# Kernel optimization log

Hardware: AMD Instinct MI355X
Metric: run time of the kernel (lower is better)

Reference implementation:

```python
import jax, jax.numpy as jnp
import numpy as np

B, N, C, H = 4, 1024, 768, 12
D = C // H
SCALE = D ** -0.5


def setup_inputs() -> dict:
    key = jax.random.key(0)
    k1, k2, k3, k4 = jax.random.split(key, 4)
    x1 = jax.random.normal(k1, (B, N, C), dtype=jnp.float32)
    x2 = jax.random.normal(k2, (B, N, C), dtype=jnp.float32)
    # shared (dual-stream) Linear2 weights, torch nn.Linear layout: [out, in]
    W_qkv = jax.random.normal(k3, (3 * C, C), dtype=jnp.float32) * (C ** -0.5)
    b_qkv = jnp.zeros((3 * C,), dtype=jnp.float32)
    W_proj = jax.random.normal(k4, (C, C), dtype=jnp.float32) * (C ** -0.5)
    b_proj = jnp.zeros((C,), dtype=jnp.float32)
    return {"x1": x1, "x2": x2, "W_qkv": W_qkv, "b_qkv": b_qkv,
            "W_proj": W_proj, "b_proj": b_proj}


def _split_qkv(x, W_qkv, b_qkv):
    qkv = (x @ W_qkv.T + b_qkv).reshape(B, N, 3, H, D)
    qkv = jnp.transpose(qkv, (2, 0, 3, 1, 4))  # [3,B,H,N,D]
    return qkv[0], qkv[1], qkv[2]


def reference(x1, x2, W_qkv, b_qkv, W_proj, b_proj):
    q1, k1, v1 = _split_qkv(x1, W_qkv, b_qkv)
    q2, k2, v2 = _split_qkv(x2, W_qkv, b_qkv)
    # two score maps, combined before a single shared softmax
    s1 = jnp.einsum("bhqd,bhkd->bhqk", q1 * SCALE, k1)
    s2 = jnp.einsum("bhqd,bhkd->bhqk", q2 * SCALE, k2)
    attn = jax.nn.softmax(s1 + s2, axis=-1)  # [B,H,N,N]
    # same attention matrix applied to both value streams
    o1 = jnp.einsum("bhqk,bhkd->bhqd", attn, v1)
    o2 = jnpum = jnp.einsum("bhqk,bhkd->bhqd", attn, v2) if False else jnp.einsum("bhqk,bhkd->bhqd", attn, v2)
    o1 = jnp.transpose(o1, (0, 2, 1, 3)).reshape(B, N, C)
    o2 = jnp.transpose(o2, (0, 2, 1, 3)).reshape(B, N, C)
    y1 = o1 @ W_proj.T + b_proj
    y2 = o2 @ W_proj.T + b_proj
    return y1, y2
```

## Files before the change

kernel.cpp:

```cpp
#include <hip/hip_runtime.h>
#include <hip/hip_bf16.h>


typedef __bf16 bf16x8 __attribute__((ext_vector_type(8)));
typedef __bf16 bf16x4 __attribute__((ext_vector_type(4)));
typedef float  f32x4  __attribute__((ext_vector_type(4)));

__device__ __forceinline__ bf16x8 cvt8(const float* p) {
    f32x4 f0 = *(const f32x4*)p;
    f32x4 f1 = *(const f32x4*)(p + 4);
    bf16x8 r;
    r[0] = (__bf16)f0[0]; r[1] = (__bf16)f0[1]; r[2] = (__bf16)f0[2]; r[3] = (__bf16)f0[3];
    r[4] = (__bf16)f1[0]; r[5] = (__bf16)f1[1]; r[6] = (__bf16)f1[2]; r[7] = (__bf16)f1[3];
    return r;
}

__device__ __forceinline__ void async16(const __bf16* g, __bf16* l) {
    __builtin_amdgcn_global_load_lds(
        (const __attribute__((address_space(1))) void*)g,
        (__attribute__((address_space(3))) void*)l, 16, 0, 0);
}

__global__ __launch_bounds__(256)
void cvt4_k(const float* __restrict__ x1, const float* __restrict__ x2,
            const float* __restrict__ wq, const float* __restrict__ wp,
            __bf16* __restrict__ xc, __bf16* __restrict__ wqc,
            __bf16* __restrict__ wpc)
{
    int bid = blockIdx.x;
    const float* src; __bf16* dst; int i;
    if (bid < 1536)      { src = x1; dst = xc;             i = (bid * 256 + threadIdx.x) * 8; }
    else if (bid < 3072) { src = x2; dst = xc + 3145728;   i = ((bid - 1536) * 256 + threadIdx.x) * 8; }
    else if (bid < 3936) { src = wq; dst = wqc;            i = ((bid - 3072) * 256 + threadIdx.x) * 8; }
    else                 { src = wp; dst = wpc;            i = ((bid - 3936) * 256 + threadIdx.x) * 8; }
    *(bf16x8*)(dst + i) = cvt8(src + i);
}

__global__ __launch_bounds__(256)
void cvt_k(const float* __restrict__ src, __bf16* __restrict__ dst, int n) {
    int i = (blockIdx.x * 256 + threadIdx.x) * 8;
    if (i < n) *(bf16x8*)(dst + i) = cvt8(src + i);
}

__global__ __launch_bounds__(256)
void gemm_qkv_s(const __bf16* __restrict__ Xc, const __bf16* __restrict__ Wq,
                const float* __restrict__ bias,
                __bf16* __restrict__ qo, __bf16* __restrict__ ko,
                __bf16* __restrict__ vo)
{
    constexpr int K = 768;
    __shared__ __bf16 As[3][128 * 32];
    __shared__ __bf16 Bs[3][128 * 32];

    const int t = threadIdx.x, w = t >> 6, lane = t & 63;
    const int l15 = lane & 15, quad = lane >> 4;
    const int wm = w >> 1, wn = w & 1;

    const int bid  = blockIdx.x;
    const int xcd  = bid & 7;
    const int i6   = bid >> 3;
    const int pair = i6 / 18;
    const int gx   = i6 - pair * 18;
    const int p    = xcd * 8 + pair;
    const int gy   = p & 31;
    const int st   = p >> 5;

    const int sgrp = w * 32;
    const int srow = lane & 15;
    const int scol = (lane >> 4) * 8;

    const __bf16* Ab = Xc + (size_t)st * 3145728 + (size_t)(gy * 128) * K;
    const __bf16* Bb = Wq + (size_t)(gx * 128) * K;

    f32x4 acc[4][4];
#pragma unroll
    for (int mi = 0; mi < 4; mi++)
#pragma unroll
        for (int ni = 0; ni < 4; ni++) acc[mi][ni] = f32x4{0.f, 0.f, 0.f, 0.f};

#define QSTAGE(BUF, KT)                                                          \
    do {                                                                         \
        const int _k0 = (KT) * 32;                                               \
        async16(Ab + (size_t)(sgrp + srow) * K + _k0 + scol,                     \
                &As[BUF][sgrp * 32 + lane * 8]);                                 \
        async16(Ab + (size_t)(sgrp + 16 + srow) * K + _k0 + scol,                \
                &As[BUF][(sgrp + 16) * 32 + lane * 8]);                          \
        async16(Bb + (size_t)(sgrp + srow) * K + _k0 + scol,                     \
                &Bs[BUF][sgrp * 32 + lane * 8]);                                 \
        async16(Bb + (size_t)(sgrp + 16 + srow) * K + _k0 + scol,                \
                &Bs[BUF][(sgrp + 16) * 32 + lane * 8]);                          \
    } while (0)

    QSTAGE(0, 0);

#pragma unroll 3
    for (int kt = 0; kt < 24; kt++) {
        const int cb = kt % 3;
        if (kt < 23) {
            QSTAGE((kt + 1) % 3, kt + 1);
            asm volatile("s_waitcnt vmcnt(4)" ::: "memory");
        } else {
            asm volatile("s_waitcnt vmcnt(0)" ::: "memory");
        }
        __builtin_amdgcn_s_barrier();
        __builtin_amdgcn_sched_barrier(0);

        bf16x8 af[4], bfr[4];
#pragma unroll
        for (int mi = 0; mi < 4; mi++)
            af[mi] = *(const bf16x8*)&As[cb][(wm * 64 + mi * 16) * 32 + lane * 8];
#pragma unroll
        for (int ni = 0; ni < 4; ni++)
            bfr[ni] = *(const bf16x8*)&Bs[cb][(wn * 64 + ni * 16) * 32 + lane * 8];
#pragma unroll
        for (int mi = 0; mi < 4; mi++)
#pragma unroll
            for (int ni = 0; ni < 4; ni++)
                acc[mi][ni] = __builtin_amdgcn_mfma_f32_16x16x32_bf16(af[mi], bfr[ni], acc[mi][ni], 0, 0, 0);
    }
#undef QSTAGE

    const int which = (gx * 128) / 768;

    if (which == 2) {
#pragma unroll
        for (int ni = 0; ni < 4; ni++) {
            int j = gx * 128 + wn * 64 + ni * 16 + l15;
            int c = j - 1536;
            int h = c >> 6, d = c & 63;
            float bj = bias[j];
#pragma unroll
            for (int mi = 0; mi < 4; mi++) {
                int row0 = gy * 128 + wm * 64 + mi * 16 + quad * 4;
                int b = row0 >> 10, tok0 = row0 & 1023;
                bf16x4 pv;
#pragma unroll
                for (int r = 0; r < 4; r++) pv[r] = (__bf16)(acc[mi][ni][r] + bj);
                *(bf16x4*)&vo[((size_t)((st * 4 + b) * 12 + h) * 64 + d) * 1024 + tok0] = pv;
            }
        }
    } else {
#pragma unroll
        for (int ni = 0; ni < 4; ni++) {
            int j     = gx * 128 + wn * 64 + ni * 16 + l15;
            int c     = j - which * 768;
            int h = c >> 6, d = c & 63;
            float bj  = bias[j];
#pragma unroll
            for (int mi = 0; mi < 4; mi++) {
#pragma unroll
                for (int r = 0; r < 4; r++) {
                    int row = gy * 128 + wm * 64 + mi * 16 + quad * 4 + r;
                    int b = row >> 10, tok = row & 1023;
                    float val = acc[mi][ni][r] + bj;
                    if (which == 0)
                        qo[((size_t)((st * 4 + b) * 12 + h) * 1024 + tok) * 64 + d] = (__bf16)(val * 0.125f);
                    else
                        ko[((size_t)((st * 4 + b) * 12 + h) * 1024 + tok) * 64 + d] = (__bf16)val;
                }
            }
        }
    }
}

__global__ __launch_bounds__(256)
void gemm_proj(const __bf16* __restrict__ A, const __bf16* __restrict__ Wp,
               const float* __restrict__ bias, float* __restrict__ out)
{
    constexpr int K = 768;
    __shared__ __bf16 As[3][128 * 32];
    __shared__ __bf16 Bs[3][128 * 32];

    const int t = threadIdx.x, w = t >> 6, lane = t & 63;
    const int l15 = lane & 15, quad = lane >> 4;
    const int wm = w >> 1, wn = w & 1;
    const int gx = blockIdx.x, gy = blockIdx.y;

    const int sgrp = w * 32;
    const int srow = lane & 15;
    const int scol = (lane >> 4) * 8;

    const __bf16* Ab = A  + (size_t)(gy * 128) * K;
    const __bf16* Bb = Wp + (size_t)(gx * 128) * K;

    f32x4 acc[4][4];
#pragma unroll
    for (int mi = 0; mi < 4; mi++)
#pragma unroll
        for (int ni = 0; ni < 4; ni++) acc[mi][ni] = f32x4{0.f, 0.f, 0.f, 0.f};

#define PSTAGE(BUF, KT)                                                          \
    do {                                                                         \
        const int _k0 = (KT) * 32;                                               \
        async16(Ab + (size_t)(sgrp + srow) * K + _k0 + scol,                     \
                &As[BUF][sgrp * 32 + lane * 8]);                                 \
        async16(Ab + (size_t)(sgrp + 16 + srow) * K + _k0 + scol,                \
                &As[BUF][(sgrp + 16) * 32 + lane * 8]);                          \
        async16(Bb + (size_t)(sgrp + srow) * K + _k0 + scol,                     \
                &Bs[BUF][sgrp * 32 + lane * 8]);                                 \
        async16(Bb + (size_t)(sgrp + 16 + srow) * K + _k0 + scol,                \
                &Bs[BUF][(sgrp + 16) * 32 + lane * 8]);                          \
    } while (0)

    PSTAGE(0, 0);

#pragma unroll 3
    for (int kt = 0; kt < 24; kt++) {
        const int cb = kt % 3;
        if (kt < 23) {
            PSTAGE((kt + 1) % 3, kt + 1);
            asm volatile("s_waitcnt vmcnt(4)" ::: "memory");
        } else {
            asm volatile("s_waitcnt vmcnt(0)" ::: "memory");
        }
        __builtin_amdgcn_s_barrier();
        __builtin_amdgcn_sched_barrier(0);

        bf16x8 af[4], bfr[4];
#pragma unroll
        for (int mi = 0; mi < 4; mi++)
            af[mi] = *(const bf16x8*)&As[cb][(wm * 64 + mi * 16) * 32 + lane * 8];
#pragma unroll
        for (int ni = 0; ni < 4; ni++)
            bfr[ni] = *(const bf16x8*)&Bs[cb][(wn * 64 + ni * 16) * 32 + lane * 8];
#pragma unroll
        for (int mi = 0; mi < 4; mi++)
#pragma unroll
            for (int ni = 0; ni < 4; ni++)
                acc[mi][ni] = __builtin_amdgcn_mfma_f32_16x16x32_bf16(af[mi], bfr[ni], acc[mi][ni], 0, 0, 0);
    }
#undef PSTAGE

#pragma unroll
    for (int ni = 0; ni < 4; ni++) {
        int col  = gx * 128 + wn * 64 + ni * 16 + l15;
        float bj = bias[col];
#pragma unroll
        for (int mi = 0; mi < 4; mi++)
#pragma unroll
            for (int r = 0; r < 4; r++) {
                int row = gy * 128 + wm * 64 + mi * 16 + quad * 4 + r;
                out[(size_t)row * 768 + col] = acc[mi][ni][r] + bj;
            }
    }
}

__global__ __launch_bounds__(128, 2)
void attn_k(const __bf16* __restrict__ qws, const __bf16* __restrict__ kws,
            const __bf16* __restrict__ vws, __bf16* __restrict__ ows)
{
    __shared__ __bf16 Ks[2][2][2][2][512];
    __shared__ __bf16 Vs[2][2][4][512];
    __shared__ __bf16 Ps[2][2][16 * 72];

    const int g  = blockIdx.x;
    const int qt = g / 48;
    const int bh = g % 48;
    const int b = bh / 12, h = bh % 12;
    const int t = threadIdx.x, w = t >> 6, lane = t & 63;
    const int l15 = lane & 15, quad = lane >> 4;

    const size_t head_off = (size_t)bh * 65536;
    const size_t ss       = (size_t)48 * 65536;

    bf16x8 qf[2][2][2];
#pragma unroll
    for (int set = 0; set < 2; set++)
#pragma unroll
        for (int s = 0; s < 2; s++)
#pragma unroll
            for (int kk = 0; kk < 2; kk++)
                qf[set][s][kk] = *(const bf16x8*)(qws + s * ss + head_off
                    + (size_t)(qt * 64 + w * 32 + set * 16 + l15) * 64 + kk * 32 + quad * 8);

    float lsum[2] = {0.f, 0.f};
    f32x4 accO[2][2][4];
#pragma unroll
    for (int set = 0; set < 2; set++)
#pragma unroll
        for (int s = 0; s < 2; s++)
#pragma unroll
            for (int mi = 0; mi < 4; mi++) accO[set][s][mi] = f32x4{0.f, 0.f, 0.f, 0.f};

    const __bf16* kbase = kws + head_off;
    const __bf16* vbase = vws + head_off;

#define STAGE_TILE(BUF, KEYB)                                                   \
    do {                                                                        \
        if (w == 0) {                                                           \
            _Pragma("unroll")                                                   \
            for (int i = 0; i < 8; i++) {                                       \
                const int s = i >> 2, kk = (i >> 1) & 1, mi = i & 1;            \
                async16(kbase + s * ss + (size_t)((KEYB) + mi * 16 + l15) * 64  \
                            + kk * 32 + quad * 8,                               \
                        &Ks[BUF][s][kk][mi][lane * 8]);                         \
            }                                                                   \
        } else {                                                                \
            _Pragma("unroll")                                                   \
            for (int i = 0; i < 8; i++) {                                       \
                const int s = i >> 2, mi = i & 3;                               \
                async16(vbase + s * ss + (size_t)(mi * 16 + l15) * 1024         \
                            + (KEYB) + quad * 8,                                \
                        &Vs[BUF][s][mi][lane * 8]);                             \
            }                                                                   \
        }                                                                       \
    } while (0)

    STAGE_TILE(0, 0);
    __syncthreads();

#pragma unroll 2
    for (int kt = 0; kt < 32; kt++) {
        const int cb = kt & 1, nb = cb ^ 1;

        if (kt < 31) STAGE_TILE(nb, (kt + 1) * 32);

        f32x4 accS[2][2];
#pragma unroll
        for (int set = 0; set < 2; set++)
#pragma unroll
            for (int mi = 0; mi < 2; mi++) accS[set][mi] = f32x4{0.f, 0.f, 0.f, 0.f};
        __builtin_amdgcn_s_setprio(1);
#pragma unroll
        for (int s = 0; s < 2; s++)
#pragma unroll
            for (int kk = 0; kk < 2; kk++) {
                bf16x8 kf0 = *(const bf16x8*)&Ks[cb][s][kk][0][lane * 8];
                bf16x8 kf1 = *(const bf16x8*)&Ks[cb][s][kk][1][lane * 8];
#pragma unroll
                for (int set = 0; set < 2; set++) {
                    accS[set][0] = __builtin_amdgcn_mfma_f32_16x16x32_bf16(kf0, qf[set][s][kk], accS[set][0], 0, 0, 0);
                    accS[set][1] = __builtin_amdgcn_mfma_f32_16x16x32_bf16(kf1, qf[set][s][kk], accS[set][1], 0, 0, 0);
                }
            }
        __builtin_amdgcn_s_setprio(0);

#pragma unroll
        for (int set = 0; set < 2; set++) {
            float rs = 0.f;
#pragma unroll
            for (int mi = 0; mi < 2; mi++) {
                bf16x4 pk;
#pragma unroll
                for (int r = 0; r < 4; r++) {
                    float pv = __expf(accS[set][mi][r]);
                    pk[r] = (__bf16)pv;
                    rs += pv;
                }
                *(bf16x4*)&Ps[w][set][l15 * 72 + mi * 16 + quad * 4] = pk;
            }
            lsum[set] += rs;
        }

        bf16x8 pa0 = *(const bf16x8*)&Ps[w][0][l15 * 72 + quad * 8];
        bf16x8 pa1 = *(const bf16x8*)&Ps[w][1][l15 * 72 + quad * 8];
        __builtin_amdgcn_s_setprio(1);
#pragma unroll
        for (int s = 0; s < 2; s++)
#pragma unroll
            for (int mi = 0; mi < 4; mi++) {
                bf16x8 vf = *(const bf16x8*)&Vs[cb][s][mi][lane * 8];
                accO[0][s][mi] = __builtin_amdgcn_mfma_f32_16x16x32_bf16(vf, pa0, accO[0][s][mi], 0, 0, 0);
                accO[1][s][mi] = __builtin_amdgcn_mfma_f32_16x16x32_bf16(vf, pa1, accO[1][s][mi], 0, 0, 0);
            }
        __builtin_amdgcn_s_setprio(0);

        __syncthreads();
    }
#undef STAGE_TILE

#pragma unroll
    for (int set = 0; set < 2; set++) {
        float l = lsum[set];
        l += __shfl_xor(l, 16);
        l += __shfl_xor(l, 32);
        float il = 1.f / l;

        const int tok = qt * 64 + w * 32 + set * 16 + l15;
#pragma unroll
        for (int s = 0; s < 2; s++)
#pragma unroll
            for (int mi = 0; mi < 4; mi++) {
                bf16x4 ov;
#pragma unroll
                for (int r = 0; r < 4; r++) ov[r] = (__bf16)(accO[set][s][mi][r] * il);
                *(bf16x4*)&ows[((size_t)((s * 4 + b) * 1024 + tok)) * 768
                               + h * 64 + mi * 16 + quad * 4] = ov;
            }
    }
}

extern "C" void kernel_launch(void* const* d_in, const int* in_sizes, int n_in,
                              void* d_out, int out_size, void* d_ws, size_t ws_size,
                              hipStream_t stream)
{
    const float* x1    = (const float*)d_in[0];
    const float* x2    = (const float*)d_in[1];
    const float* Wqkv  = (const float*)d_in[2];
    const float* bqkv  = (const float*)d_in[3];
    const float* Wproj = (const float*)d_in[4];
    const float* bproj = (const float*)d_in[5];
    float* out = (float*)d_out;

    const size_t qkv_elems = (size_t)2 * 4 * 12 * 1024 * 64;
    __bf16* q_ws = (__bf16*)d_ws;
    __bf16* k_ws = q_ws + qkv_elems;
    __bf16* v_ws = k_ws + qkv_elems;
    __bf16* pool = v_ws + qkv_elems;
    __bf16* Wqc  = pool + 3145728;
    __bf16* o_ws = pool;
    __bf16* Xc   = (__bf16*)d_out;

    const bool big = ws_size >= (size_t)(4 * qkv_elems + 589824) * sizeof(__bf16);
    __bf16* Wpc = big ? (pool + qkv_elems)
                      : q_ws;

    cvt4_k<<<big ? 4224 : 3936, 256, 0, stream>>>(x1, x2, Wqkv, Wproj, Xc, Wqc, Wpc);
    gemm_qkv_s<<<1152, 256, 0, stream>>>(Xc, Wqc, bqkv, q_ws, k_ws, v_ws);
    attn_k<<<768, 128, 0, stream>>>(q_ws, k_ws, v_ws, o_ws);
    if (!big) cvt_k<<<288, 256, 0, stream>>>(Wproj, Wpc, 589824);
    gemm_proj<<<dim3(6, 64), 256, 0, stream>>>(o_ws, Wpc, bproj, out);
}
```

Measured before the change: 238.0 us.

## Pre-tile bf16 GEMM operands so each async LDS load is contiguous

The conversion kernels now write X, W_qkv and W_proj in a tiled layout of 16-row by 32-column blocks, ordered to match the LDS staging order. The attention kernel writes its output in the same tiled layout. With that layout, each wave's global_load_lds in both GEMMs reads one contiguous 1 KB chunk instead of 16 strided row segments. This is meant to improve global memory coalescing during GEMM staging, at the cost of more index arithmetic in the conversion kernels and a scattered store pattern in the attention epilogue.

New measurement: 208.3 us. -12.4%, faster.

```diff
diff --git a/kernel.cpp b/kernel.cpp
--- a/kernel.cpp
+++ b/kernel.cpp
@@ -21,6 +21,17 @@
         (__attribute__((address_space(3))) void*)l, 16, 0, 0);
 }
 
+__device__ __forceinline__ void cvt_tiled_one(const float* __restrict__ src,
+                                              __bf16* __restrict__ dst, int j) {
+    const int r  = j & 15;
+    const int ks = (j >> 4) & 3;
+    const int t2 = j >> 6;
+    const int kt = t2 % 24;
+    const int G  = t2 / 24;
+    *(bf16x8*)(dst + (size_t)j * 8) =
+        cvt8(src + (size_t)(G * 16 + r) * 768 + kt * 32 + ks * 8);
+}
+
 __global__ __launch_bounds__(256)
 void cvt4_k(const float* __restrict__ x1, const float* __restrict__ x2,
             const float* __restrict__ wq, const float* __restrict__ wp,
@@ -28,18 +39,16 @@
             __bf16* __restrict__ wpc)
 {
     int bid = blockIdx.x;
-    const float* src; __bf16* dst; int i;
-    if (bid < 1536)      { src = x1; dst = xc;             i = (bid * 256 + threadIdx.x) * 8; }
-    else if (bid < 3072) { src = x2; dst = xc + 3145728;   i = ((bid - 1536) * 256 + threadIdx.x) * 8; }
-    else if (bid < 3936) { src = wq; dst = wqc;            i = ((bid - 3072) * 256 + threadIdx.x) * 8; }
-    else                 { src = wp; dst = wpc;            i = ((bid - 3936) * 256 + threadIdx.x) * 8; }
-    *(bf16x8*)(dst + i) = cvt8(src + i);
+    if (bid < 1536)      cvt_tiled_one(x1, xc,            bid * 256 + threadIdx.x);
+    else if (bid < 3072) cvt_tiled_one(x2, xc + 3145728, (bid - 1536) * 256 + threadIdx.x);
+    else if (bid < 3936) cvt_tiled_one(wq, wqc,          (bid - 3072) * 256 + threadIdx.x);
+    else                 cvt_tiled_one(wp, wpc,          (bid - 3936) * 256 + threadIdx.x);
 }
 
 __global__ __launch_bounds__(256)
-void cvt_k(const float* __restrict__ src, __bf16* __restrict__ dst, int n) {
-    int i = (blockIdx.x * 256 + threadIdx.x) * 8;
-    if (i < n) *(bf16x8*)(dst + i) = cvt8(src + i);
+void cvt_kt(const float* __restrict__ src, __bf16* __restrict__ dst, int nrun) {
+    int j = blockIdx.x * 256 + threadIdx.x;
+    if (j < nrun) cvt_tiled_one(src, dst, j);
 }
 
 __global__ __launch_bounds__(256)
@@ -48,7 +57,6 @@
                 __bf16* __restrict__ qo, __bf16* __restrict__ ko,
                 __bf16* __restrict__ vo)
 {
-    constexpr int K = 768;
     __shared__ __bf16 As[3][128 * 32];
     __shared__ __bf16 Bs[3][128 * 32];
 
@@ -65,30 +73,27 @@
     const int gy   = p & 31;
     const int st   = p >> 5;
 
-    const int sgrp = w * 32;
-    const int srow = lane & 15;
-    const int scol = (lane >> 4) * 8;
-
-    const __bf16* Ab = Xc + (size_t)st * 3145728 + (size_t)(gy * 128) * K;
-    const __bf16* Bb = Wq + (size_t)(gx * 128) * K;
+    const __bf16* Ab = Xc + (size_t)st * 3145728 + (size_t)(gy * 8) * 24 * 512;
+    const __bf16* Bb = Wq + (size_t)(gx * 8) * 24 * 512;
 
     f32x4 acc[4][4];
 #pragma unroll
     for (int mi = 0; mi < 4; mi++)
 #pragma unroll
         for (int ni = 0; ni < 4; ni++) acc[mi][ni] = f32x4{0.f, 0.f, 0.f, 0.f};
+
+    const int ga0 = w * 2, ga1 = w * 2 + 1;
 
 #define QSTAGE(BUF, KT)                                                          \
     do {                                                                         \
-        const int _k0 = (KT) * 32;                                               \
-        async16(Ab + (size_t)(sgrp + srow) * K + _k0 + scol,                     \
-                &As[BUF][sgrp * 32 + lane * 8]);                                 \
-        async16(Ab + (size_t)(sgrp + 16 + srow) * K + _k0 + scol,                \
-                &As[BUF][(sgrp + 16) * 32 + lane * 8]);                          \
-        async16(Bb + (size_t)(sgrp + srow) * K + _k0 + scol,                     \
-                &Bs[BUF][sgrp * 32 + lane * 8]);                                 \
-        async16(Bb + (size_t)(sgrp + 16 + srow) * K + _k0 + scol,                \
-                &Bs[BUF][(sgrp + 16) * 32 + lane * 8]);                          \
+        async16(Ab + ((size_t)ga0 * 24 + (KT)) * 512 + lane * 8,                 \
+                &As[BUF][ga0 * 512 + lane * 8]);                                 \
+        async16(Ab + ((size_t)ga1 * 24 + (KT)) * 512 + lane * 8,                 \
+                &As[BUF][ga1 * 512 + lane * 8]);                                 \
+        async16(Bb + ((size_t)ga0 * 24 + (KT)) * 512 + lane * 8,                 \
+                &Bs[BUF][ga0 * 512 + lane * 8]);                                 \
+        async16(Bb + ((size_t)ga1 * 24 + (KT)) * 512 + lane * 8,                 \
+                &Bs[BUF][ga1 * 512 + lane * 8]);                                 \
     } while (0)
 
     QSTAGE(0, 0);
@@ -108,10 +113,10 @@
         bf16x8 af[4], bfr[4];
 #pragma unroll
         for (int mi = 0; mi < 4; mi++)
-            af[mi] = *(const bf16x8*)&As[cb][(wm * 64 + mi * 16) * 32 + lane * 8];
+            af[mi] = *(const bf16x8*)&As[cb][(wm * 4 + mi) * 512 + lane * 8];
 #pragma unroll
         for (int ni = 0; ni < 4; ni++)
-            bfr[ni] = *(const bf16x8*)&Bs[cb][(wn * 64 + ni * 16) * 32 + lane * 8];
+            bfr[ni] = *(const bf16x8*)&Bs[cb][(wn * 4 + ni) * 512 + lane * 8];
 #pragma unroll
         for (int mi = 0; mi < 4; mi++)
 #pragma unroll
@@ -167,7 +172,6 @@
 void gemm_proj(const __bf16* __restrict__ A, const __bf16* __restrict__ Wp,
                const float* __restrict__ bias, float* __restrict__ out)
 {
-    constexpr int K = 768;
     __shared__ __bf16 As[3][128 * 32];
     __shared__ __bf16 Bs[3][128 * 32];
 
@@ -176,30 +180,27 @@
     const int wm = w >> 1, wn = w & 1;
     const int gx = blockIdx.x, gy = blockIdx.y;
 
-    const int sgrp = w * 32;
-    const int srow = lane & 15;
-    const int scol = (lane >> 4) * 8;
-
-    const __bf16* Ab = A  + (size_t)(gy * 128) * K;
-    const __bf16* Bb = Wp + (size_t)(gx * 128) * K;
+    const __bf16* Ab = A  + (size_t)(gy * 8) * 24 * 512;
+    const __bf16* Bb = Wp + (size_t)(gx * 8) * 24 * 512;
 
     f32x4 acc[4][4];
 #pragma unroll
     for (int mi = 0; mi < 4; mi++)
 #pragma unroll
         for (int ni = 0; ni < 4; ni++) acc[mi][ni] = f32x4{0.f, 0.f, 0.f, 0.f};
+
+    const int ga0 = w * 2, ga1 = w * 2 + 1;
 
 #define PSTAGE(BUF, KT)                                                          \
     do {                                                                         \
-        const int _k0 = (KT) * 32;                                               \
-        async16(Ab + (size_t)(sgrp + srow) * K + _k0 + scol,                     \
-                &As[BUF][sgrp * 32 + lane * 8]);                                 \
-        async16(Ab + (size_t)(sgrp + 16 + srow) * K + _k0 + scol,                \
-                &As[BUF][(sgrp + 16) * 32 + lane * 8]);                          \
-        async16(Bb + (size_t)(sgrp + srow) * K + _k0 + scol,                     \
-                &Bs[BUF][sgrp * 32 + lane * 8]);                                 \
-        async16(Bb + (size_t)(sgrp + 16 + srow) * K + _k0 + scol,                \
-                &Bs[BUF][(sgrp + 16) * 32 + lane * 8]);                          \
+        async16(Ab + ((size_t)ga0 * 24 + (KT)) * 512 + lane * 8,                 \
+                &As[BUF][ga0 * 512 + lane * 8]);                                 \
+        async16(Ab + ((size_t)ga1 * 24 + (KT)) * 512 + lane * 8,                 \
+                &As[BUF][ga1 * 512 + lane * 8]);                                 \
+        async16(Bb + ((size_t)ga0 * 24 + (KT)) * 512 + lane * 8,                 \
+                &Bs[BUF][ga0 * 512 + lane * 8]);                                 \
+        async16(Bb + ((size_t)ga1 * 24 + (KT)) * 512 + lane * 8,                 \
+                &Bs[BUF][ga1 * 512 + lane * 8]);                                 \
     } while (0)
 
     PSTAGE(0, 0);
@@ -219,10 +220,10 @@
         bf16x8 af[4], bfr[4];
 #pragma unroll
         for (int mi = 0; mi < 4; mi++)
-            af[mi] = *(const bf16x8*)&As[cb][(wm * 64 + mi * 16) * 32 + lane * 8];
+            af[mi] = *(const bf16x8*)&As[cb][(wm * 4 + mi) * 512 + lane * 8];
 #pragma unroll
         for (int ni = 0; ni < 4; ni++)
-            bfr[ni] = *(const bf16x8*)&Bs[cb][(wn * 64 + ni * 16) * 32 + lane * 8];
+            bfr[ni] = *(const bf16x8*)&Bs[cb][(wn * 4 + ni) * 512 + lane * 8];
 #pragma unroll
         for (int mi = 0; mi < 4; mi++)
 #pragma unroll
@@ -384,8 +385,11 @@
                 bf16x4 ov;
 #pragma unroll
                 for (int r = 0; r < 4; r++) ov[r] = (__bf16)(accO[set][s][mi][r] * il);
-                *(bf16x4*)&ows[((size_t)((s * 4 + b) * 1024 + tok)) * 768
-                               + h * 64 + mi * 16 + quad * 4] = ov;
+                const int row = (s * 4 + b) * 1024 + tok;
+                const int c   = h * 64 + mi * 16 + quad * 4;
+                const size_t off = ((size_t)(row >> 4) * 24 + (c >> 5)) * 512
+                                 + ((c >> 3) & 3) * 128 + (row & 15) * 8 + (c & 7);
+                *(bf16x4*)&ows[off] = ov;
             }
     }
 }
@@ -418,6 +422,6 @@
     cvt4_k<<<big ? 4224 : 3936, 256, 0, stream>>>(x1, x2, Wqkv, Wproj, Xc, Wqc, Wpc);
     gemm_qkv_s<<<1152, 256, 0, stream>>>(Xc, Wqc, bqkv, q_ws, k_ws, v_ws);
     attn_k<<<768, 128, 0, stream>>>(q_ws, k_ws, v_ws, o_ws);
-    if (!big) cvt_k<<<288, 256, 0, stream>>>(Wproj, Wpc, 589824);
+    if (!big) cvt_kt<<<288, 256, 0, stream>>>(Wproj, Wpc, 73728);
     gemm_proj<<<dim3(6, 64), 256, 0, stream>>>(o_ws, Wpc, bproj, out);
 }
```
